# Optimization experiments

Hardware: AMD Instinct MI355X
Metric: run time of the kernel (lower is better)

Reference implementation:

```python
import jax, jax.numpy as jnp
import numpy as np


def setup_inputs() -> dict:
    key = jax.random.key(0)
    k1, k2 = jax.random.split(key)
    # (C, N, 2) projected circle points; only circle 0 is used
    img_render_points = jax.random.normal(k1, (2, 4096, 2), dtype=jnp.float32) * 100.0
    # (K, M, 2) skeleton slices; only the last slice is used
    ref_catheter_skeleton = jax.random.normal(k2, (2, 32768, 2), dtype=jnp.float32) * 100.0
    return {"img_render_points": img_render_points,
            "ref_catheter_skeleton": ref_catheter_skeleton}


def reference(img_render_points, ref_catheter_skeleton):
    # first projected circle -> (N, 2)
    pts = img_render_points[0].reshape(-1, 2)
    # last skeleton slice, point order flipped (flip is math-neutral for chamfer) -> (M, 2)
    ref = ref_catheter_skeleton[-1][::-1]
    # pairwise Euclidean distances (N, M) via the squared-norm expansion
    # ||a-b||^2 = ||a||^2 + ||b||^2 - 2 a.b  (avoids materializing (N, M, 2))
    sq = (jnp.sum(pts * pts, axis=1)[:, None]
          + jnp.sum(ref * ref, axis=1)[None, :]
          - 2.0 * (pts @ ref.T))
    dist = jnp.sqrt(jnp.maximum(sq, 1e-12))  # (N, M)
    chamfer = jnp.sum(jnp.min(dist, axis=1)) + jnp.sum(jnp.min(dist, axis=0))
    return chamfer
```

## Files before the change

kernel.cpp:

```cpp
#include <hip/hip_runtime.h>


typedef float v2f __attribute__((ext_vector_type(2)));

constexpr int N_PTS = 4096;
constexpr int M_REF = 32768;
constexpr int P_OWN = 16;
constexpr int S_STG = 128;
constexpr int R_SLC = 256;
constexpr int C_SLC = 32;

__global__ __launch_bounds__(256) void chamfer_main_kernel(
    const float2* __restrict__ pts, const float2* __restrict__ refs,
    float* __restrict__ rowpart,
    float* __restrict__ colpart)
{
    __shared__ float4 sxy[S_STG / 2];
    __shared__ float2 sz [S_STG / 2];
    const int tid = threadIdx.x, b = blockIdx.x;

    const float2* own; const float2* oth; float* part;
    int ownBase, sbase;
    if (b < 256) {
        own = pts;  oth = refs;
        ownBase = tid * P_OWN;
        sbase   = b * S_STG;
        part    = rowpart + b * N_PTS + ownBase;
    } else {
        const int bb = b - 256;
        own = refs; oth = pts;
        ownBase = (bb & 7) * 4096 + tid * P_OWN;
        sbase   = (bb >> 3) * S_STG;
        part    = colpart + (bb >> 3) * M_REF + ownBase;
    }

    if (tid < S_STG / 2) {
        const float4 rr = ((const float4*)(oth + sbase))[tid];
        sxy[tid] = make_float4(-2.f * rr.x, -2.f * rr.z, -2.f * rr.y, -2.f * rr.w);
        sz [tid] = make_float2(fmaf(rr.x, rr.x, rr.y * rr.y),
                               fmaf(rr.z, rr.z, rr.w * rr.w));
    }

    v2f px2[P_OWN], py2[P_OWN];
    float mn[P_OWN];
    {
        const float4* o4 = (const float4*)(own + ownBase);
        #pragma unroll
        for (int q = 0; q < P_OWN / 2; ++q) {
            const float4 o = o4[q];
            px2[2 * q]     = (v2f){o.x, o.x}; py2[2 * q]     = (v2f){o.y, o.y};
            px2[2 * q + 1] = (v2f){o.z, o.z}; py2[2 * q + 1] = (v2f){o.w, o.w};
        }
        #pragma unroll
        for (int k = 0; k < P_OWN; ++k) mn[k] = 3.0e38f;
    }
    __syncthreads();

    for (int j = 0; j < S_STG / 2; ++j) {
        const float4 xy = sxy[j];
        const float2 zz = sz[j];
        const v2f rx2 = (v2f){xy.x, xy.y};
        const v2f ry2 = (v2f){xy.z, xy.w};
        const v2f rz2 = (v2f){zz.x, zz.y};
        #pragma unroll
        for (int k = 0; k < P_OWN; ++k) {
            const v2f d2 = px2[k] * rx2 + (py2[k] * ry2 + rz2);
            mn[k] = fminf(fminf(mn[k], d2.x), d2.y);
        }
    }

    float4* w = (float4*)part;
    #pragma unroll
    for (int q = 0; q < P_OWN / 4; ++q)
        w[q] = make_float4(mn[4 * q], mn[4 * q + 1], mn[4 * q + 2], mn[4 * q + 3]);
}

__global__ __launch_bounds__(256) void chamfer_fold_kernel(
    const float2* __restrict__ pts, const float2* __restrict__ refs,
    const float4* __restrict__ rowpart4,
    const float4* __restrict__ colpart4,
    float* __restrict__ partial)
{
    __shared__ float4 red[256];
    __shared__ float ssum[4];
    const int tid = threadIdx.x, b = blockIdx.x;
    float dsum = 0.f;

    if (b < 32) {
        const int lane = tid & 31, sc = tid >> 5;
        const int f4 = b * 32 + lane;
        float4 m = rowpart4[(sc * 32) * (N_PTS / 4) + f4];
        for (int s = 1; s < 32; ++s) {
            const float4 v = rowpart4[(sc * 32 + s) * (N_PTS / 4) + f4];
            m.x = fminf(m.x, v.x); m.y = fminf(m.y, v.y);
            m.z = fminf(m.z, v.z); m.w = fminf(m.w, v.w);
        }
        red[sc * 32 + lane] = m;
        __syncthreads();
        if (tid < 32) {
            float4 mm = red[tid];
            #pragma unroll
            for (int c = 1; c < 8; ++c) {
                const float4 v = red[c * 32 + tid];
                mm.x = fminf(mm.x, v.x); mm.y = fminf(mm.y, v.y);
                mm.z = fminf(mm.z, v.z); mm.w = fminf(mm.w, v.w);
            }
            const int f4g = b * 32 + tid;
            const float4 pa = ((const float4*)pts)[2 * f4g];
            const float4 pb = ((const float4*)pts)[2 * f4g + 1];
            dsum = sqrtf(fmaxf(mm.x + fmaf(pa.x, pa.x, pa.y * pa.y), 1e-12f))
                 + sqrtf(fmaxf(mm.y + fmaf(pa.z, pa.z, pa.w * pa.w), 1e-12f))
                 + sqrtf(fmaxf(mm.z + fmaf(pb.x, pb.x, pb.y * pb.y), 1e-12f))
                 + sqrtf(fmaxf(mm.w + fmaf(pb.z, pb.z, pb.w * pb.w), 1e-12f));
        }
    } else {
        const int cb = b - 32;
        const int lane = tid & 127, sc = tid >> 7;
        const int f4 = cb * 128 + lane;
        float4 m = colpart4[(sc * 16) * (M_REF / 4) + f4];
        for (int s = 1; s < 16; ++s) {
            const float4 v = colpart4[(sc * 16 + s) * (M_REF / 4) + f4];
            m.x = fminf(m.x, v.x); m.y = fminf(m.y, v.y);
            m.z = fminf(m.z, v.z); m.w = fminf(m.w, v.w);
        }
        red[sc * 128 + lane] = m;
        __syncthreads();
        if (tid < 128) {
            float4 mm = red[tid];
            const float4 v = red[128 + tid];
            mm.x = fminf(mm.x, v.x); mm.y = fminf(mm.y, v.y);
            mm.z = fminf(mm.z, v.z); mm.w = fminf(mm.w, v.w);
            const int f4g = cb * 128 + tid;
            const float4 ra = ((const float4*)refs)[2 * f4g];
            const float4 rb = ((const float4*)refs)[2 * f4g + 1];
            dsum = sqrtf(fmaxf(mm.x + fmaf(ra.x, ra.x, ra.y * ra.y), 1e-12f))
                 + sqrtf(fmaxf(mm.y + fmaf(ra.z, ra.z, ra.w * ra.w), 1e-12f))
                 + sqrtf(fmaxf(mm.z + fmaf(rb.x, rb.x, rb.y * rb.y), 1e-12f))
                 + sqrtf(fmaxf(mm.w + fmaf(rb.z, rb.z, rb.w * rb.w), 1e-12f));
        }
    }

    #pragma unroll
    for (int off = 32; off > 0; off >>= 1) dsum += __shfl_down(dsum, off, 64);
    const int lane = tid & 63, wave = tid >> 6;
    if (lane == 0) ssum[wave] = dsum;
    __syncthreads();
    if (tid == 0) partial[b] = ssum[0] + ssum[1] + ssum[2] + ssum[3];
}

__global__ __launch_bounds__(128) void chamfer_final_kernel(
    const float* __restrict__ partial, float* __restrict__ out)
{
    __shared__ float ssum[2];
    const int tid = threadIdx.x;
    float d = (tid < 96) ? partial[tid] : 0.f;
    #pragma unroll
    for (int off = 32; off > 0; off >>= 1) d += __shfl_down(d, off, 64);
    const int lane = tid & 63, wave = tid >> 6;
    if (lane == 0) ssum[wave] = d;
    __syncthreads();
    if (tid == 0) out[0] = ssum[0] + ssum[1];
}

extern "C" void kernel_launch(void* const* d_in, const int* in_sizes, int n_in,
                              void* d_out, int out_size, void* d_ws, size_t ws_size,
                              hipStream_t stream) {
    const float2* pts  = (const float2*)d_in[0];
    const float2* refs = ((const float2*)d_in[1]) + M_REF;

    float* rowpart = (float*)d_ws;
    float* colpart = rowpart + R_SLC * N_PTS;
    float* partial = colpart + C_SLC * M_REF;
    float* out = (float*)d_out;

    chamfer_main_kernel <<<512, 256, 0, stream>>>(pts, refs, rowpart, colpart);
    chamfer_fold_kernel <<<96, 256, 0, stream>>>(pts, refs,
                                                 (const float4*)rowpart,
                                                 (const float4*)colpart, partial);
    chamfer_final_kernel<<<1, 128, 0, stream>>>(partial, out);
}
```

Measured before the change: 34.74 us.

## Fuse three kernels into one persistent kernel with software grid barriers

```diff
diff --git a/kernel.cpp b/kernel.cpp
--- a/kernel.cpp
+++ b/kernel.cpp
@@ -9,157 +9,175 @@
 constexpr int S_STG = 128;
 constexpr int R_SLC = 256;
 constexpr int C_SLC = 32;
+constexpr unsigned int NBLK = 512;
 
-__global__ __launch_bounds__(256) void chamfer_main_kernel(
+__device__ __forceinline__ void grid_barrier(unsigned int* counter)
+{
+    __syncthreads();
+    if (threadIdx.x == 0) {
+        __threadfence();
+        atomicAdd(counter, 1u);
+        while (__hip_atomic_load(counter, __ATOMIC_RELAXED,
+                                 __HIP_MEMORY_SCOPE_AGENT) < NBLK) {
+            __builtin_amdgcn_s_sleep(2);
+        }
+        __threadfence();
+    }
+    __syncthreads();
+}
+
+__global__ __launch_bounds__(256, 2) void chamfer_fused_kernel(
     const float2* __restrict__ pts, const float2* __restrict__ refs,
     float* __restrict__ rowpart,
-    float* __restrict__ colpart)
+    float* __restrict__ colpart,
+    float* __restrict__ partial,
+    unsigned int* __restrict__ counters,
+    float* __restrict__ out)
 {
     __shared__ float4 sxy[S_STG / 2];
     __shared__ float2 sz [S_STG / 2];
+    __shared__ float4 red[256];
+    __shared__ float  ssum[4];
     const int tid = threadIdx.x, b = blockIdx.x;
 
-    const float2* own; const float2* oth; float* part;
-    int ownBase, sbase;
-    if (b < 256) {
-        own = pts;  oth = refs;
-        ownBase = tid * P_OWN;
-        sbase   = b * S_STG;
-        part    = rowpart + b * N_PTS + ownBase;
-    } else {
-        const int bb = b - 256;
-        own = refs; oth = pts;
-        ownBase = (bb & 7) * 4096 + tid * P_OWN;
-        sbase   = (bb >> 3) * S_STG;
-        part    = colpart + (bb >> 3) * M_REF + ownBase;
+    {
+        const float2* own; const float2* oth; float* part;
+        int ownBase, sbase;
+        if (b < 256) {
+            own = pts;  oth = refs;
+            ownBase = tid * P_OWN;
+            sbase   = b * S_STG;
+            part    = rowpart + b * N_PTS + ownBase;
+        } else {
+            const int bb = b - 256;
+            own = refs; oth = pts;
+            ownBase = (bb & 7) * 4096 + tid * P_OWN;
+            sbase   = (bb >> 3) * S_STG;
+            part    = colpart + (bb >> 3) * M_REF + ownBase;
+        }
+
+        if (tid < S_STG / 2) {
+            const float4 rr = ((const float4*)(oth + sbase))[tid];
+            sxy[tid] = make_float4(-2.f * rr.x, -2.f * rr.z, -2.f * rr.y, -2.f * rr.w);
+            sz [tid] = make_float2(fmaf(rr.x, rr.x, rr.y * rr.y),
+                                   fmaf(rr.z, rr.z, rr.w * rr.w));
+        }
+
+        v2f px2[P_OWN], py2[P_OWN];
+        float mn[P_OWN];
+        {
+            const float4* o4 = (const float4*)(own + ownBase);
+            #pragma unroll
+            for (int q = 0; q < P_OWN / 2; ++q) {
+                const float4 o = o4[q];
+                px2[2 * q]     = (v2f){o.x, o.x}; py2[2 * q]     = (v2f){o.y, o.y};
+                px2[2 * q + 1] = (v2f){o.z, o.z}; py2[2 * q + 1] = (v2f){o.w, o.w};
+            }
+            #pragma unroll
+            for (int k = 0; k < P_OWN; ++k) mn[k] = 3.0e38f;
+        }
+        __syncthreads();
+
+        #pragma unroll 2
+        for (int j = 0; j < S_STG / 2; ++j) {
+            const float4 xy = sxy[j];
+            const float2 zz = sz[j];
+            const v2f rx2 = (v2f){xy.x, xy.y};
+            const v2f ry2 = (v2f){xy.z, xy.w};
+            const v2f rz2 = (v2f){zz.x, zz.y};
+            #pragma unroll
+            for (int k = 0; k < P_OWN; ++k) {
+                const v2f d2 = px2[k] * rx2 + (py2[k] * ry2 + rz2);
+                mn[k] = fminf(fminf(mn[k], d2.x), d2.y);
+            }
+        }
+
+        float4* w = (float4*)part;
+        #pragma unroll
+        for (int q = 0; q < P_OWN / 4; ++q)
+            w[q] = make_float4(mn[4 * q], mn[4 * q + 1], mn[4 * q + 2], mn[4 * q + 3]);
     }
 
-    if (tid < S_STG / 2) {
-        const float4 rr = ((const float4*)(oth + sbase))[tid];
-        sxy[tid] = make_float4(-2.f * rr.x, -2.f * rr.z, -2.f * rr.y, -2.f * rr.w);
-        sz [tid] = make_float2(fmaf(rr.x, rr.x, rr.y * rr.y),
-                               fmaf(rr.z, rr.z, rr.w * rr.w));
+    grid_barrier(&counters[0]);
+
+    if (b < 96) {
+        const float4* rowpart4 = (const float4*)rowpart;
+        const float4* colpart4 = (const float4*)colpart;
+        float dsum = 0.f;
+
+        if (b < 32) {
+            const int lane = tid & 31, sc = tid >> 5;
+            const int f4 = b * 32 + lane;
+            float4 m = rowpart4[(sc * 32) * (N_PTS / 4) + f4];
+            for (int s = 1; s < 32; ++s) {
+                const float4 v = rowpart4[(sc * 32 + s) * (N_PTS / 4) + f4];
+                m.x = fminf(m.x, v.x); m.y = fminf(m.y, v.y);
+                m.z = fminf(m.z, v.z); m.w = fminf(m.w, v.w);
+            }
+            red[sc * 32 + lane] = m;
+            __syncthreads();
+            if (tid < 32) {
+                float4 mm = red[tid];
+                #pragma unroll
+                for (int c = 1; c < 8; ++c) {
+                    const float4 v = red[c * 32 + tid];
+                    mm.x = fminf(mm.x, v.x); mm.y = fminf(mm.y, v.y);
+                    mm.z = fminf(mm.z, v.z); mm.w = fminf(mm.w, v.w);
+                }
+                const int f4g = b * 32 + tid;
+                const float4 pa = ((const float4*)pts)[2 * f4g];
+                const float4 pb = ((const float4*)pts)[2 * f4g + 1];
+                dsum = sqrtf(fmaxf(mm.x + fmaf(pa.x, pa.x, pa.y * pa.y), 1e-12f))
+                     + sqrtf(fmaxf(mm.y + fmaf(pa.z, pa.z, pa.w * pa.w), 1e-12f))
+                     + sqrtf(fmaxf(mm.z + fmaf(pb.x, pb.x, pb.y * pb.y), 1e-12f))
+                     + sqrtf(fmaxf(mm.w + fmaf(pb.z, pb.z, pb.w * pb.w), 1e-12f));
+            }
+        } else {
+            const int cb = b - 32;
+            const int lane = tid & 127, sc = tid >> 7;
+            const int f4 = cb * 128 + lane;
+            float4 m = colpart4[(sc * 16) * (M_REF / 4) + f4];
+            for (int s = 1; s < 16; ++s) {
+                const float4 v = colpart4[(sc * 16 + s) * (M_REF / 4) + f4];
+                m.x = fminf(m.x, v.x); m.y = fminf(m.y, v.y);
+                m.z = fminf(m.z, v.z); m.w = fminf(m.w, v.w);
+            }
+            red[sc * 128 + lane] = m;
+            __syncthreads();
+            if (tid < 128) {
+                float4 mm = red[tid];
+                const float4 v = red[128 + tid];
+                mm.x = fminf(mm.x, v.x); mm.y = fminf(mm.y, v.y);
+                mm.z = fminf(mm.z, v.z); mm.w = fminf(mm.w, v.w);
+                const int f4g = cb * 128 + tid;
+                const float4 ra = ((const float4*)refs)[2 * f4g];
+                const float4 rb = ((const float4*)refs)[2 * f4g + 1];
+                dsum = sqrtf(fmaxf(mm.x + fmaf(ra.x, ra.x, ra.y * ra.y), 1e-12f))
+                     + sqrtf(fmaxf(mm.y + fmaf(ra.z, ra.z, ra.w * ra.w), 1e-12f))
+                     + sqrtf(fmaxf(mm.z + fmaf(rb.x, rb.x, rb.y * rb.y), 1e-12f))
+                     + sqrtf(fmaxf(mm.w + fmaf(rb.z, rb.z, rb.w * rb.w), 1e-12f));
+            }
+        }
+
+        #pragma unroll
+        for (int off = 32; off > 0; off >>= 1) dsum += __shfl_down(dsum, off, 64);
+        const int lane = tid & 63, wave = tid >> 6;
+        if (lane == 0) ssum[wave] = dsum;
+        __syncthreads();
+        if (tid == 0) partial[b] = ssum[0] + ssum[1] + ssum[2] + ssum[3];
     }
 
-    v2f px2[P_OWN], py2[P_OWN];
-    float mn[P_OWN];
-    {
-        const float4* o4 = (const float4*)(own + ownBase);
+    grid_barrier(&counters[1]);
+
+    if (b == 0) {
+        float d = (tid < 96) ? partial[tid] : 0.f;
         #pragma unroll
-        for (int q = 0; q < P_OWN / 2; ++q) {
-            const float4 o = o4[q];
-            px2[2 * q]     = (v2f){o.x, o.x}; py2[2 * q]     = (v2f){o.y, o.y};
-            px2[2 * q + 1] = (v2f){o.z, o.z}; py2[2 * q + 1] = (v2f){o.w, o.w};
-        }
-        #pragma unroll
-        for (int k = 0; k < P_OWN; ++k) mn[k] = 3.0e38f;
+        for (int off = 32; off > 0; off >>= 1) d += __shfl_down(d, off, 64);
+        const int lane = tid & 63, wave = tid >> 6;
+        if (lane == 0) ssum[wave] = d;
+        __syncthreads();
+        if (tid == 0) out[0] = ssum[0] + ssum[1] + ssum[2] + ssum[3];
     }
-    __syncthreads();
-
-    for (int j = 0; j < S_STG / 2; ++j) {
-        const float4 xy = sxy[j];
-        const float2 zz = sz[j];
-        const v2f rx2 = (v2f){xy.x, xy.y};
-        const v2f ry2 = (v2f){xy.z, xy.w};
-        const v2f rz2 = (v2f){zz.x, zz.y};
-        #pragma unroll
-        for (int k = 0; k < P_OWN; ++k) {
-            const v2f d2 = px2[k] * rx2 + (py2[k] * ry2 + rz2);
-            mn[k] = fminf(fminf(mn[k], d2.x), d2.y);
-        }
-    }
-
-    float4* w = (float4*)part;
-    #pragma unroll
-    for (int q = 0; q < P_OWN / 4; ++q)
-        w[q] = make_float4(mn[4 * q], mn[4 * q + 1], mn[4 * q + 2], mn[4 * q + 3]);
-}
-
-__global__ __launch_bounds__(256) void chamfer_fold_kernel(
-    const float2* __restrict__ pts, const float2* __restrict__ refs,
-    const float4* __restrict__ rowpart4,
-    const float4* __restrict__ colpart4,
-    float* __restrict__ partial)
-{
-    __shared__ float4 red[256];
-    __shared__ float ssum[4];
-    const int tid = threadIdx.x, b = blockIdx.x;
-    float dsum = 0.f;
-
-    if (b < 32) {
-        const int lane = tid & 31, sc = tid >> 5;
-        const int f4 = b * 32 + lane;
-        float4 m = rowpart4[(sc * 32) * (N_PTS / 4) + f4];
-        for (int s = 1; s < 32; ++s) {
-            const float4 v = rowpart4[(sc * 32 + s) * (N_PTS / 4) + f4];
-            m.x = fminf(m.x, v.x); m.y = fminf(m.y, v.y);
-            m.z = fminf(m.z, v.z); m.w = fminf(m.w, v.w);
-        }
-        red[sc * 32 + lane] = m;
-        __syncthreads();
-        if (tid < 32) {
-            float4 mm = red[tid];
-            #pragma unroll
-            for (int c = 1; c < 8; ++c) {
-                const float4 v = red[c * 32 + tid];
-                mm.x = fminf(mm.x, v.x); mm.y = fminf(mm.y, v.y);
-                mm.z = fminf(mm.z, v.z); mm.w = fminf(mm.w, v.w);
-            }
-            const int f4g = b * 32 + tid;
-            const float4 pa = ((const float4*)pts)[2 * f4g];
-            const float4 pb = ((const float4*)pts)[2 * f4g + 1];
-            dsum = sqrtf(fmaxf(mm.x + fmaf(pa.x, pa.x, pa.y * pa.y), 1e-12f))
-                 + sqrtf(fmaxf(mm.y + fmaf(pa.z, pa.z, pa.w * pa.w), 1e-12f))
-                 + sqrtf(fmaxf(mm.z + fmaf(pb.x, pb.x, pb.y * pb.y), 1e-12f))
-                 + sqrtf(fmaxf(mm.w + fmaf(pb.z, pb.z, pb.w * pb.w), 1e-12f));
-        }
-    } else {
-        const int cb = b - 32;
-        const int lane = tid & 127, sc = tid >> 7;
-        const int f4 = cb * 128 + lane;
-        float4 m = colpart4[(sc * 16) * (M_REF / 4) + f4];
-        for (int s = 1; s < 16; ++s) {
-            const float4 v = colpart4[(sc * 16 + s) * (M_REF / 4) + f4];
-            m.x = fminf(m.x, v.x); m.y = fminf(m.y, v.y);
-            m.z = fminf(m.z, v.z); m.w = fminf(m.w, v.w);
-        }
-        red[sc * 128 + lane] = m;
-        __syncthreads();
-        if (tid < 128) {
-            float4 mm = red[tid];
-            const float4 v = red[128 + tid];
-            mm.x = fminf(mm.x, v.x); mm.y = fminf(mm.y, v.y);
-            mm.z = fminf(mm.z, v.z); mm.w = fminf(mm.w, v.w);
-            const int f4g = cb * 128 + tid;
-            const float4 ra = ((const float4*)refs)[2 * f4g];
-            const float4 rb = ((const float4*)refs)[2 * f4g + 1];
-            dsum = sqrtf(fmaxf(mm.x + fmaf(ra.x, ra.x, ra.y * ra.y), 1e-12f))
-                 + sqrtf(fmaxf(mm.y + fmaf(ra.z, ra.z, ra.w * ra.w), 1e-12f))
-                 + sqrtf(fmaxf(mm.z + fmaf(rb.x, rb.x, rb.y * rb.y), 1e-12f))
-                 + sqrtf(fmaxf(mm.w + fmaf(rb.z, rb.z, rb.w * rb.w), 1e-12f));
-        }
-    }
-
-    #pragma unroll
-    for (int off = 32; off > 0; off >>= 1) dsum += __shfl_down(dsum, off, 64);
-    const int lane = tid & 63, wave = tid >> 6;
-    if (lane == 0) ssum[wave] = dsum;
-    __syncthreads();
-    if (tid == 0) partial[b] = ssum[0] + ssum[1] + ssum[2] + ssum[3];
-}
-
-__global__ __launch_bounds__(128) void chamfer_final_kernel(
-    const float* __restrict__ partial, float* __restrict__ out)
-{
-    __shared__ float ssum[2];
-    const int tid = threadIdx.x;
-    float d = (tid < 96) ? partial[tid] : 0.f;
-    #pragma unroll
-    for (int off = 32; off > 0; off >>= 1) d += __shfl_down(d, off, 64);
-    const int lane = tid & 63, wave = tid >> 6;
-    if (lane == 0) ssum[wave] = d;
-    __syncthreads();
-    if (tid == 0) out[0] = ssum[0] + ssum[1];
 }
 
 extern "C" void kernel_launch(void* const* d_in, const int* in_sizes, int n_in,
@@ -171,11 +189,10 @@
     float* rowpart = (float*)d_ws;
     float* colpart = rowpart + R_SLC * N_PTS;
     float* partial = colpart + C_SLC * M_REF;
+    unsigned int* counters = (unsigned int*)(partial + 96);
     float* out = (float*)d_out;
 
-    chamfer_main_kernel <<<512, 256, 0, stream>>>(pts, refs, rowpart, colpart);
-    chamfer_fold_kernel <<<96, 256, 0, stream>>>(pts, refs,
-                                                 (const float4*)rowpart,
-                                                 (const float4*)colpart, partial);
-    chamfer_final_kernel<<<1, 128, 0, stream>>>(partial, out);
+    hipMemsetAsync(counters, 0, 2 * sizeof(unsigned int), stream);
+    chamfer_fused_kernel<<<NBLK, 256, 0, stream>>>(pts, refs, rowpart, colpart,
+                                                   partial, counters, out);
 }
```

After: 133.3 us. +283.8%, slower.
